# Kernel optimization log

Hardware: AMD Instinct MI355X
Metric: run time of the kernel (lower is better)

Reference implementation:

```python
import jax, jax.numpy as jnp
import numpy as np

EMBED_DIM = 1280
NUM_HEADS = 16
HEAD_DIM = EMBED_DIM // NUM_HEADS  # 80
SCALE = HEAD_DIM ** -0.5
BATCH = 16
SEQ = 1024


def setup_inputs() -> dict:
    key = jax.random.key(0)
    k1, k2, k3, k4, k5 = jax.random.split(key, 5)
    return {
        "hidden_states": jax.random.normal(k1, (BATCH, SEQ, EMBED_DIM), dtype=jnp.float32),
        "w_qkv": jax.random.normal(k2, (EMBED_DIM, 3 * EMBED_DIM), dtype=jnp.float32) * (EMBED_DIM ** -0.5),
        "b_qkv": jax.random.normal(k3, (3 * EMBED_DIM,), dtype=jnp.float32) * 0.02,
        "w_proj": jax.random.normal(k4, (EMBED_DIM, EMBED_DIM), dtype=jnp.float32) * (EMBED_DIM ** -0.5),
        "b_proj": jax.random.normal(k5, (EMBED_DIM,), dtype=jnp.float32) * 0.02,
    }


def reference(hidden_states, w_qkv, b_qkv, w_proj, b_proj):
    b, s, e = hidden_states.shape
    # QKV projection: [b, s, 3e] -> [3, b, h, s, d]
    qkv = hidden_states @ w_qkv + b_qkv
    qkv = qkv.reshape(b, s, 3, NUM_HEADS, HEAD_DIM).transpose(2, 0, 3, 1, 4)
    q, k, v = qkv[0], qkv[1], qkv[2]
    # full attention matrix [b, h, s, s]
    attn = jnp.einsum("bhqd,bhkd->bhqk", q, k) * SCALE
    attn = jax.nn.softmax(attn, axis=-1)
    # dropout p=0.0 (eval): identity
    out = jnp.einsum("bhqk,bhkd->bhqd", attn, v)
    out = out.transpose(0, 2, 1, 3).reshape(b, s, e)
    return out @ w_proj + b_proj
```

## Files before the change

kernel.cpp:

```cpp
#include <hip/hip_runtime.h>

#define BATCH 16
#define SEQ   1024
#define EMBED 1280
#define NH    16
#define HD    80
#define HDP   96
#define NQKV  3840
#define MTOK  (BATCH*SEQ)
#define SCALE 0.11180339887498948f
#define LOG2E 1.4426950408889634f

#define SK_STRIDE 104
#define SV_STRIDE 72
#define SP_STRIDE 72

typedef _Float16 half8 __attribute__((ext_vector_type(8)));
typedef _Float16 half4 __attribute__((ext_vector_type(4)));
typedef float floatx4 __attribute__((ext_vector_type(4)));

#define GLD_TO_LDS(gp, lp)                                                        \
  __builtin_amdgcn_global_load_lds(                                               \
      (const __attribute__((address_space(1))) void*)(gp),                        \
      (__attribute__((address_space(3))) void*)(lp), 16, 0, 0)

__device__ __forceinline__ float rowmax16(float x) {
#define DPP_MAX(ctrl)                                                             \
  {                                                                               \
    float y = __int_as_float(                                                     \
        __builtin_amdgcn_update_dpp(0, __float_as_int(x), ctrl, 0xF, 0xF, true)); \
    x = fmaxf(x, y);                                                              \
  }
  DPP_MAX(0xB1);
  DPP_MAX(0x4E);
  DPP_MAX(0x141);
  DPP_MAX(0x140);
#undef DPP_MAX
  return x;
}

__global__ void cvt_f32_to_f16(const float4* __restrict__ in, _Float16* __restrict__ out, int n4) {
  int i = blockIdx.x * blockDim.x + threadIdx.x;
  if (i < n4) {
    float4 v = in[i];
    half4 h;
    h[0] = (_Float16)v.x; h[1] = (_Float16)v.y; h[2] = (_Float16)v.z; h[3] = (_Float16)v.w;
    *(half4*)(out + (size_t)i * 4) = h;
  }
}

template <int N>
__global__ void cvt_transpose_f16(const float* __restrict__ in, _Float16* __restrict__ out) {
  __shared__ float tile[32][33];
  const int tx = threadIdx.x & 31, ty = threadIdx.x >> 5;
  const int k0 = blockIdx.y * 32;
  const int n0 = blockIdx.x * 32;
#pragma unroll
  for (int j = 0; j < 4; ++j)
    tile[ty + 8 * j][tx] = in[(size_t)(k0 + ty + 8 * j) * N + n0 + tx];
  __syncthreads();
#pragma unroll
  for (int j = 0; j < 4; ++j)
    out[(size_t)(n0 + ty + 8 * j) * 1280 + k0 + tx] = (_Float16)tile[tx][ty + 8 * j];
}


#define STAGE_A(H, T, D)                                                           \
  do {                                                                             \
    GLD_TO_LDS(aSrc0 + (size_t)((H) * 128) * 1280 + (T) * 64,                      \
               &sA[D][((H) * 128 + wave * 16) * 64]);                              \
    GLD_TO_LDS(aSrc0 + (size_t)((H) * 128 + 8) * 1280 + (T) * 64,                  \
               &sA[D][((H) * 128 + wave * 16 + 8) * 64]);                          \
  } while (0)

#define STAGE_B(H, T, D)                                                           \
  do {                                                                             \
    GLD_TO_LDS(bSrc0 + (size_t)((H) * 128) * 1280 + (T) * 64,                      \
               &sB[D][((H) * 128 + wave * 16) * 64]);                              \
    GLD_TO_LDS(bSrc0 + (size_t)((H) * 128 + 8) * 1280 + (T) * 64,                  \
               &sB[D][((H) * 128 + wave * 16 + 8) * 64]);                          \
  } while (0)

#define LDS_FRAG(P, ROWB, FR, KK) (*(const half8*)((P) + ((ROWB) + (FR) * 16) * 64 + cofs[KK]))

#define MFMA_Q(MIB, NIB)                                                           \
  _Pragma("unroll") for (int mi = 0; mi < 4; ++mi)                                 \
    _Pragma("unroll") for (int ni = 0; ni < 2; ++ni)                               \
      _Pragma("unroll") for (int kk = 0; kk < 2; ++kk)                             \
        acc[(MIB) + mi][(NIB) + ni] = __builtin_amdgcn_mfma_f32_16x16x32_f16(      \
            af[mi][kk], bf[(NIB) + ni][kk], acc[(MIB) + mi][(NIB) + ni], 0, 0, 0)

#define GBODY(T, D, S1, S2, VNSTR)                                                 \
  {                                                                                \
    const _Float16* pA = &sA[D][0];                                                \
    const _Float16* pB = &sB[D][0];                                                \
                         \
    _Pragma("unroll") for (int mi = 0; mi < 4; ++mi)                               \
      _Pragma("unroll") for (int kk = 0; kk < 2; ++kk)                             \
        af[mi][kk] = LDS_FRAG(pA, rA, mi, kk);                                     \
    _Pragma("unroll") for (int ni = 0; ni < 2; ++ni)                               \
      _Pragma("unroll") for (int kk = 0; kk < 2; ++kk)                             \
        bf[ni][kk] = LDS_FRAG(pB, rB, ni, kk);                                     \
    if (S1) { STAGE_A(1, (T) + 1, (D) ^ 1); }                                      \
    __builtin_amdgcn_s_barrier();                                                  \
    asm volatile("s_waitcnt lgkmcnt(0)" ::: "memory");                             \
    __builtin_amdgcn_s_setprio(1);                                                 \
    MFMA_Q(0, 0);                                                                  \
    __builtin_amdgcn_s_setprio(0);                                                 \
    __builtin_amdgcn_s_barrier();                                                  \
                                                   \
    _Pragma("unroll") for (int ni = 0; ni < 2; ++ni)                               \
      _Pragma("unroll") for (int kk = 0; kk < 2; ++kk)                             \
        bf[2 + ni][kk] = LDS_FRAG(pB, rB, 2 + ni, kk);                             \
    __builtin_amdgcn_s_barrier();                                                  \
    asm volatile("s_waitcnt lgkmcnt(0)" ::: "memory");                             \
    __builtin_amdgcn_s_setprio(1);                                                 \
    MFMA_Q(0, 2);                                                                  \
    __builtin_amdgcn_s_setprio(0);                                                 \
    __builtin_amdgcn_s_barrier();                                                  \
                                  \
    _Pragma("unroll") for (int mi = 0; mi < 4; ++mi)                               \
      _Pragma("unroll") for (int kk = 0; kk < 2; ++kk)                             \
        af[mi][kk] = LDS_FRAG(pA, rA, 4 + mi, kk);                                 \
    if (S2) { STAGE_B(0, (T) + 2, (D)); }                                          \
    __builtin_amdgcn_s_barrier();                                                  \
    asm volatile("s_waitcnt lgkmcnt(0)" ::: "memory");                             \
    __builtin_amdgcn_s_setprio(1);                                                 \
    MFMA_Q(4, 0);                                                                  \
    __builtin_amdgcn_s_setprio(0);                                                 \
    __builtin_amdgcn_s_barrier();                                                  \
            \
    if (S2) { STAGE_A(0, (T) + 2, (D)); STAGE_B(1, (T) + 2, (D)); }                \
    __builtin_amdgcn_s_barrier();                                                  \
    __builtin_amdgcn_s_setprio(1);                                                 \
    MFMA_Q(4, 2);                                                                  \
    __builtin_amdgcn_s_setprio(0);                                                 \
    asm volatile("s_waitcnt " VNSTR ::: "memory");                                 \
    __builtin_amdgcn_s_barrier();                                                  \
  }

template <int MODE>
__global__ __launch_bounds__(512, 2)
void gemm256(const _Float16* __restrict__ A, const _Float16* __restrict__ Bt,
             const float* __restrict__ bias,
             _Float16* __restrict__ q_pad, _Float16* __restrict__ k_pad,
             _Float16* __restrict__ v_t, float* __restrict__ outf) {
  __shared__ __align__(16) _Float16 sA[2][256 * 64];
  __shared__ __align__(16) _Float16 sB[2][256 * 64];

  const int tid = threadIdx.x;
  const int wave = tid >> 6, lane = tid & 63, quad = lane >> 4, r16 = lane & 15;
  const int wm = wave >> 2, wn = wave & 3;

  const int pid = blockIdx.x;
  const int xcd = pid & 7, local = pid >> 3;
  const int mt = xcd * 8 + (local & 7);
  const int nt = local >> 3;
  const int m0 = mt * 256, n0 = nt * 256;

  const int l8 = lane >> 3, cg = (lane & 7) ^ l8;
  const _Float16* aSrc0 = A + ((size_t)m0 + wave * 16 + l8) * 1280 + cg * 8;
  const _Float16* bSrc0 = Bt + ((size_t)n0 + wave * 16 + l8) * 1280 + cg * 8;

  const int rA = wm * 128 + r16;
  const int rB = wn * 64 + r16;
  const int cofs[2] = { ((0 + quad) ^ (r16 & 7)) * 8, ((4 + quad) ^ (r16 & 7)) * 8 };

  floatx4 acc[8][4] = {};
  half8 af[4][2], bf[4][2];

  STAGE_A(0, 0, 0); STAGE_A(1, 0, 0); STAGE_B(0, 0, 0); STAGE_B(1, 0, 0);
  STAGE_B(0, 1, 1); STAGE_A(0, 1, 1); STAGE_B(1, 1, 1);
  asm volatile("s_waitcnt vmcnt(6)" ::: "memory");
  __builtin_amdgcn_s_barrier();

  for (int it = 0; it < 9; ++it) {
    GBODY(2 * it, 0, true, true, "vmcnt(6)");
    GBODY(2 * it + 1, 1, true, true, "vmcnt(6)");
  }
  GBODY(18, 0, true, false, "vmcnt(0)");
  GBODY(19, 1, false, false, "vmcnt(0)");

  if (MODE == 1) {
#pragma unroll
    for (int mi = 0; mi < 8; ++mi)
#pragma unroll
      for (int ni = 0; ni < 4; ++ni) {
        int n = n0 + wn * 64 + ni * 16 + r16;
        float bv = bias[n];
#pragma unroll
        for (int r = 0; r < 4; ++r) {
          int m = m0 + wm * 128 + mi * 16 + quad * 4 + r;
          outf[(size_t)m * EMBED + n] = acc[mi][ni][r] + bv;
        }
      }
  } else {
#pragma unroll
    for (int mi = 0; mi < 8; ++mi)
#pragma unroll
      for (int ni = 0; ni < 4; ++ni) {
        int n = n0 + wn * 64 + ni * 16 + r16;
        float bv = bias[n];
        int which = n / 1280;
        int rem = n - which * 1280;
        int h = rem / 80;
        int d = rem - h * 80;
#pragma unroll
        for (int r = 0; r < 4; ++r) {
          int m = m0 + wm * 128 + mi * 16 + quad * 4 + r;
          int b = m >> 10, s = m & 1023;
          int bh = b * NH + h;
          _Float16 val = (_Float16)(acc[mi][ni][r] + bv);
          if (which == 0) {
            q_pad[((size_t)bh * SEQ + s) * HDP + d] = val;
            if (d < 16) q_pad[((size_t)bh * SEQ + s) * HDP + 80 + d] = (_Float16)0.f;
          } else if (which == 1) {
            k_pad[((size_t)bh * SEQ + s) * HDP + d] = val;
            if (d < 16) k_pad[((size_t)bh * SEQ + s) * HDP + 80 + d] = (_Float16)0.f;
          } else {
            v_t[((size_t)bh * HD + d) * SEQ + s] = val;
          }
        }
      }
  }
}

__global__ __launch_bounds__(256, 2)
void attn_kernel(const _Float16* __restrict__ q_pad, const _Float16* __restrict__ k_pad,
                 const _Float16* __restrict__ v_t, _Float16* __restrict__ attn_out) {
  __shared__ __align__(16) _Float16 sK[64 * SK_STRIDE];
  __shared__ __align__(16) _Float16 sV[96 * SV_STRIDE];
  __shared__ __align__(16) _Float16 sP[4][16 * SP_STRIDE];

  const int tid = threadIdx.x;
  const int wave = tid >> 6, lane = tid & 63, quad = lane >> 4, r16 = lane & 15;
  const int bh = blockIdx.x >> 3;
  const int q0 = (blockIdx.x & 7) * 128;

  if (tid < 128) {
    int row = 80 + (tid >> 3), col = (tid & 7) * 8;
    half8 z;
#pragma unroll
    for (int j = 0; j < 8; ++j) z[j] = (row == 80) ? (_Float16)1.f : (_Float16)0.f;
    *(half8*)(sV + row * SV_STRIDE + col) = z;
  }

  half8 qf[2][3];
#pragma unroll
  for (int mi = 0; mi < 2; ++mi) {
    const _Float16* qb = q_pad + ((size_t)bh * SEQ + q0 + wave * 32 + mi * 16 + r16) * HDP;
#pragma unroll
    for (int kq = 0; kq < 3; ++kq) {
      half8 q = *(const half8*)(qb + kq * 32 + quad * 8);
#pragma unroll
      for (int j = 0; j < 8; ++j) q[j] = q[j] * (_Float16)(SCALE * LOG2E);
      qf[mi][kq] = q;
    }
  }

  int rowK[3], colK[3];
#pragma unroll
  for (int i = 0; i < 3; ++i) {
    int c = tid + i * 256;
    rowK[i] = c / 12; colK[i] = c - rowK[i] * 12;
  }
  const int rowV0 = tid >> 3, colV0 = tid & 7;
  const _Float16* kgb = k_pad + ((size_t)bh * SEQ) * HDP;
  const _Float16* vgb = v_t + (size_t)bh * HD * SEQ;

  floatx4 o[2][6] = {};
  float mrow[2][4];
#pragma unroll
  for (int mi = 0; mi < 2; ++mi)
#pragma unroll
    for (int r = 0; r < 4; ++r) mrow[mi][r] = -1e30f;

  for (int kt = 0; kt < 16; ++kt) {
    __syncthreads();
    {
      uint4 tk0 = *(const uint4*)(kgb + ((size_t)(kt * 64 + rowK[0])) * HDP + colK[0] * 8);
      uint4 tk1 = *(const uint4*)(kgb + ((size_t)(kt * 64 + rowK[1])) * HDP + colK[1] * 8);
      uint4 tk2 = *(const uint4*)(kgb + ((size_t)(kt * 64 + rowK[2])) * HDP + colK[2] * 8);
      uint4 tv0 = *(const uint4*)(vgb + (size_t)(rowV0) * SEQ + kt * 64 + colV0 * 8);
      uint4 tv1 = *(const uint4*)(vgb + (size_t)(rowV0 + 32) * SEQ + kt * 64 + colV0 * 8);
      uint4 tv2;
      if (tid < 128)
        tv2 = *(const uint4*)(vgb + (size_t)(rowV0 + 64) * SEQ + kt * 64 + colV0 * 8);
      *(uint4*)(sK + rowK[0] * SK_STRIDE + colK[0] * 8) = tk0;
      *(uint4*)(sK + rowK[1] * SK_STRIDE + colK[1] * 8) = tk1;
      *(uint4*)(sK + rowK[2] * SK_STRIDE + colK[2] * 8) = tk2;
      *(uint4*)(sV + (rowV0) * SV_STRIDE + colV0 * 8) = tv0;
      *(uint4*)(sV + (rowV0 + 32) * SV_STRIDE + colV0 * 8) = tv1;
      if (tid < 128)
        *(uint4*)(sV + (rowV0 + 64) * SV_STRIDE + colV0 * 8) = tv2;
    }
    __syncthreads();

    floatx4 sacc[2][4] = {};
#pragma unroll
    for (int ni = 0; ni < 4; ++ni)
#pragma unroll
      for (int kq = 0; kq < 3; ++kq) {
        half8 kf = *(const half8*)(sK + (ni * 16 + r16) * SK_STRIDE + kq * 32 + quad * 8);
#pragma unroll
        for (int mi = 0; mi < 2; ++mi)
          sacc[mi][ni] = __builtin_amdgcn_mfma_f32_16x16x32_f16(qf[mi][kq], kf, sacc[mi][ni], 0, 0, 0);
      }

#pragma unroll
    for (int mi = 0; mi < 2; ++mi)
#pragma unroll
      for (int r = 0; r < 4; ++r) {
        float mx = fmaxf(fmaxf(sacc[mi][0][r], sacc[mi][1][r]),
                         fmaxf(sacc[mi][2][r], sacc[mi][3][r]));
        mx = rowmax16(mx);
        float mnew = fmaxf(mrow[mi][r], mx);
        float alpha = __builtin_amdgcn_exp2f(mrow[mi][r] - mnew);
        mrow[mi][r] = mnew;
#pragma unroll
        for (int ni = 0; ni < 4; ++ni)
          sacc[mi][ni][r] = __builtin_amdgcn_exp2f(sacc[mi][ni][r] - mnew);
#pragma unroll
        for (int di = 0; di < 6; ++di) o[mi][di][r] *= alpha;
      }

#pragma unroll
    for (int mi = 0; mi < 2; ++mi) {
#pragma unroll
      for (int ni = 0; ni < 4; ++ni)
#pragma unroll
        for (int r = 0; r < 4; ++r)
          sP[wave][(quad * 4 + r) * SP_STRIDE + ni * 16 + r16] = (_Float16)sacc[mi][ni][r];
#pragma unroll
      for (int kp = 0; kp < 2; ++kp) {
        half8 pf = *(const half8*)(&sP[wave][r16 * SP_STRIDE + kp * 32 + quad * 8]);
#pragma unroll
        for (int di = 0; di < 6; ++di) {
          half8 vf = *(const half8*)(sV + (di * 16 + r16) * SV_STRIDE + kp * 32 + quad * 8);
          o[mi][di] = __builtin_amdgcn_mfma_f32_16x16x32_f16(pf, vf, o[mi][di], 0, 0, 0);
        }
      }
    }
  }

  const int b = bh >> 4, h = bh & 15;
#pragma unroll
  for (int mi = 0; mi < 2; ++mi)
#pragma unroll
    for (int r = 0; r < 4; ++r) {
      float l = __shfl(o[mi][5][r], lane & 48);
      float inv = 1.0f / l;
      int tok = b * SEQ + q0 + wave * 32 + mi * 16 + quad * 4 + r;
#pragma unroll
      for (int di = 0; di < 5; ++di) {
        int e = h * HD + di * 16 + r16;
        attn_out[(size_t)tok * EMBED + e] = (_Float16)(o[mi][di][r] * inv);
      }
    }
}

extern "C" void kernel_launch(void* const* d_in, const int* in_sizes, int n_in,
                              void* d_out, int out_size, void* d_ws, size_t ws_size,
                              hipStream_t stream) {
  const float* hidden = (const float*)d_in[0];
  const float* w_qkv  = (const float*)d_in[1];
  const float* b_qkv  = (const float*)d_in[2];
  const float* w_proj = (const float*)d_in[3];
  const float* b_proj = (const float*)d_in[4];
  float* out = (float*)d_out;

  char* ws = (char*)d_ws;
  size_t off = 0;
  _Float16* hidden_h = (_Float16*)(ws + off); off += (size_t)MTOK * EMBED * 2;
  _Float16* wqkv_t   = (_Float16*)(ws + off); off += (size_t)NQKV * EMBED * 2;
  _Float16* wproj_t  = (_Float16*)(ws + off); off += (size_t)EMBED * EMBED * 2;
  _Float16* q_pad    = (_Float16*)(ws + off); off += (size_t)BATCH * NH * SEQ * HDP * 2;
  _Float16* k_pad    = (_Float16*)(ws + off); off += (size_t)BATCH * NH * SEQ * HDP * 2;
  _Float16* v_t      = (_Float16*)(ws + off); off += (size_t)BATCH * NH * HD * SEQ * 2;
  _Float16* attn_out = hidden_h;

  {
    int n4 = MTOK * EMBED / 4;
    cvt_f32_to_f16<<<(n4 + 255) / 256, 256, 0, stream>>>((const float4*)hidden, hidden_h, n4);
  }
  cvt_transpose_f16<NQKV><<<dim3(NQKV / 32, 1280 / 32), 256, 0, stream>>>(w_qkv, wqkv_t);
  cvt_transpose_f16<EMBED><<<dim3(EMBED / 32, 1280 / 32), 256, 0, stream>>>(w_proj, wproj_t);

  gemm256<0><<<960, 512, 0, stream>>>(hidden_h, wqkv_t, b_qkv, q_pad, k_pad, v_t, nullptr);

  attn_kernel<<<BATCH * NH * (SEQ / 128), 256, 0, stream>>>(q_pad, k_pad, v_t, attn_out);

  gemm256<1><<<320, 512, 0, stream>>>(attn_out, wproj_t, b_proj, nullptr, nullptr, nullptr, out);
}
```

Baseline: 650.3 us.

## Double-buffer K/V tiles in attention and drop extra GEMM barriers

The attention kernel now keeps two LDS buffers for K and V and prefetches the next tile into registers while the current tile's QK^T MFMAs run. The prefetched tile is written to the other buffer before the softmax, so each iteration needs one __syncthreads instead of two. The GEMM main loop drops several s_barrier and lgkmcnt waits between MFMA quarters, and s_setprio hints are added around the attention MFMAs. Removing the GEMM barriers risks LDS races if the earlier waits were needed for correctness. The extra LDS buffers may also reduce attention occupancy.

```diff
diff --git a/kernel.cpp b/kernel.cpp
--- a/kernel.cpp
+++ b/kernel.cpp
@@ -102,8 +102,6 @@
       _Pragma("unroll") for (int kk = 0; kk < 2; ++kk)                             \
         bf[ni][kk] = LDS_FRAG(pB, rB, ni, kk);                                     \
     if (S1) { STAGE_A(1, (T) + 1, (D) ^ 1); }                                      \
-    __builtin_amdgcn_s_barrier();                                                  \
-    asm volatile("s_waitcnt lgkmcnt(0)" ::: "memory");                             \
     __builtin_amdgcn_s_setprio(1);                                                 \
     MFMA_Q(0, 0);                                                                  \
     __builtin_amdgcn_s_setprio(0);                                                 \
@@ -112,8 +110,6 @@
     _Pragma("unroll") for (int ni = 0; ni < 2; ++ni)                               \
       _Pragma("unroll") for (int kk = 0; kk < 2; ++kk)                             \
         bf[2 + ni][kk] = LDS_FRAG(pB, rB, 2 + ni, kk);                             \
-    __builtin_amdgcn_s_barrier();                                                  \
-    asm volatile("s_waitcnt lgkmcnt(0)" ::: "memory");                             \
     __builtin_amdgcn_s_setprio(1);                                                 \
     MFMA_Q(0, 2);                                                                  \
     __builtin_amdgcn_s_setprio(0);                                                 \
@@ -123,15 +119,12 @@
       _Pragma("unroll") for (int kk = 0; kk < 2; ++kk)                             \
         af[mi][kk] = LDS_FRAG(pA, rA, 4 + mi, kk);                                 \
     if (S2) { STAGE_B(0, (T) + 2, (D)); }                                          \
-    __builtin_amdgcn_s_barrier();                                                  \
-    asm volatile("s_waitcnt lgkmcnt(0)" ::: "memory");                             \
     __builtin_amdgcn_s_setprio(1);                                                 \
     MFMA_Q(4, 0);                                                                  \
     __builtin_amdgcn_s_setprio(0);                                                 \
     __builtin_amdgcn_s_barrier();                                                  \
-            \
+                 \
     if (S2) { STAGE_A(0, (T) + 2, (D)); STAGE_B(1, (T) + 2, (D)); }                \
-    __builtin_amdgcn_s_barrier();                                                  \
     __builtin_amdgcn_s_setprio(1);                                                 \
     MFMA_Q(4, 2);                                                                  \
     __builtin_amdgcn_s_setprio(0);                                                 \
@@ -228,8 +221,8 @@
 __global__ __launch_bounds__(256, 2)
 void attn_kernel(const _Float16* __restrict__ q_pad, const _Float16* __restrict__ k_pad,
                  const _Float16* __restrict__ v_t, _Float16* __restrict__ attn_out) {
-  __shared__ __align__(16) _Float16 sK[64 * SK_STRIDE];
-  __shared__ __align__(16) _Float16 sV[96 * SV_STRIDE];
+  __shared__ __align__(16) _Float16 sK[2][64 * SK_STRIDE];
+  __shared__ __align__(16) _Float16 sV[2][96 * SV_STRIDE];
   __shared__ __align__(16) _Float16 sP[4][16 * SP_STRIDE];
 
   const int tid = threadIdx.x;
@@ -242,7 +235,8 @@
     half8 z;
 #pragma unroll
     for (int j = 0; j < 8; ++j) z[j] = (row == 80) ? (_Float16)1.f : (_Float16)0.f;
-    *(half8*)(sV + row * SV_STRIDE + col) = z;
+    *(half8*)(&sV[0][row * SV_STRIDE + col]) = z;
+    *(half8*)(&sV[1][row * SV_STRIDE + col]) = z;
   }
 
   half8 qf[2][3];
@@ -268,6 +262,23 @@
   const _Float16* kgb = k_pad + ((size_t)bh * SEQ) * HDP;
   const _Float16* vgb = v_t + (size_t)bh * HD * SEQ;
 
+  {
+    uint4 tk0 = *(const uint4*)(kgb + (size_t)(rowK[0]) * HDP + colK[0] * 8);
+    uint4 tk1 = *(const uint4*)(kgb + (size_t)(rowK[1]) * HDP + colK[1] * 8);
+    uint4 tk2 = *(const uint4*)(kgb + (size_t)(rowK[2]) * HDP + colK[2] * 8);
+    uint4 tv0 = *(const uint4*)(vgb + (size_t)(rowV0) * SEQ + colV0 * 8);
+    uint4 tv1 = *(const uint4*)(vgb + (size_t)(rowV0 + 32) * SEQ + colV0 * 8);
+    *(uint4*)(&sK[0][rowK[0] * SK_STRIDE + colK[0] * 8]) = tk0;
+    *(uint4*)(&sK[0][rowK[1] * SK_STRIDE + colK[1] * 8]) = tk1;
+    *(uint4*)(&sK[0][rowK[2] * SK_STRIDE + colK[2] * 8]) = tk2;
+    *(uint4*)(&sV[0][(rowV0)*SV_STRIDE + colV0 * 8]) = tv0;
+    *(uint4*)(&sV[0][(rowV0 + 32) * SV_STRIDE + colV0 * 8]) = tv1;
+    if (tid < 128) {
+      uint4 tv2 = *(const uint4*)(vgb + (size_t)(rowV0 + 64) * SEQ + colV0 * 8);
+      *(uint4*)(&sV[0][(rowV0 + 64) * SV_STRIDE + colV0 * 8]) = tv2;
+    }
+  }
+
   floatx4 o[2][6] = {};
   float mrow[2][4];
 #pragma unroll
@@ -275,37 +286,45 @@
 #pragma unroll
     for (int r = 0; r < 4; ++r) mrow[mi][r] = -1e30f;
 
+  __syncthreads();
+
   for (int kt = 0; kt < 16; ++kt) {
-    __syncthreads();
-    {
-      uint4 tk0 = *(const uint4*)(kgb + ((size_t)(kt * 64 + rowK[0])) * HDP + colK[0] * 8);
-      uint4 tk1 = *(const uint4*)(kgb + ((size_t)(kt * 64 + rowK[1])) * HDP + colK[1] * 8);
-      uint4 tk2 = *(const uint4*)(kgb + ((size_t)(kt * 64 + rowK[2])) * HDP + colK[2] * 8);
-      uint4 tv0 = *(const uint4*)(vgb + (size_t)(rowV0) * SEQ + kt * 64 + colV0 * 8);
-      uint4 tv1 = *(const uint4*)(vgb + (size_t)(rowV0 + 32) * SEQ + kt * 64 + colV0 * 8);
-      uint4 tv2;
+    const int cur = kt & 1, nxt = cur ^ 1;
+
+    uint4 tk0, tk1, tk2, tv0, tv1, tv2;
+    if (kt < 15) {
+      const int kb = (kt + 1) * 64;
+      tk0 = *(const uint4*)(kgb + (size_t)(kb + rowK[0]) * HDP + colK[0] * 8);
+      tk1 = *(const uint4*)(kgb + (size_t)(kb + rowK[1]) * HDP + colK[1] * 8);
+      tk2 = *(const uint4*)(kgb + (size_t)(kb + rowK[2]) * HDP + colK[2] * 8);
+      tv0 = *(const uint4*)(vgb + (size_t)(rowV0)*SEQ + kb + colV0 * 8);
+      tv1 = *(const uint4*)(vgb + (size_t)(rowV0 + 32) * SEQ + kb + colV0 * 8);
       if (tid < 128)
-        tv2 = *(const uint4*)(vgb + (size_t)(rowV0 + 64) * SEQ + kt * 64 + colV0 * 8);
-      *(uint4*)(sK + rowK[0] * SK_STRIDE + colK[0] * 8) = tk0;
-      *(uint4*)(sK + rowK[1] * SK_STRIDE + colK[1] * 8) = tk1;
-      *(uint4*)(sK + rowK[2] * SK_STRIDE + colK[2] * 8) = tk2;
-      *(uint4*)(sV + (rowV0) * SV_STRIDE + colV0 * 8) = tv0;
-      *(uint4*)(sV + (rowV0 + 32) * SV_STRIDE + colV0 * 8) = tv1;
-      if (tid < 128)
-        *(uint4*)(sV + (rowV0 + 64) * SV_STRIDE + colV0 * 8) = tv2;
-    }
-    __syncthreads();
+        tv2 = *(const uint4*)(vgb + (size_t)(rowV0 + 64) * SEQ + kb + colV0 * 8);
+    }
 
     floatx4 sacc[2][4] = {};
+    __builtin_amdgcn_s_setprio(1);
 #pragma unroll
     for (int ni = 0; ni < 4; ++ni)
 #pragma unroll
       for (int kq = 0; kq < 3; ++kq) {
-        half8 kf = *(const half8*)(sK + (ni * 16 + r16) * SK_STRIDE + kq * 32 + quad * 8);
+        half8 kf = *(const half8*)(&sK[cur][(ni * 16 + r16) * SK_STRIDE + kq * 32 + quad * 8]);
 #pragma unroll
         for (int mi = 0; mi < 2; ++mi)
           sacc[mi][ni] = __builtin_amdgcn_mfma_f32_16x16x32_f16(qf[mi][kq], kf, sacc[mi][ni], 0, 0, 0);
       }
+    __builtin_amdgcn_s_setprio(0);
+
+    if (kt < 15) {
+      *(uint4*)(&sK[nxt][rowK[0] * SK_STRIDE + colK[0] * 8]) = tk0;
+      *(uint4*)(&sK[nxt][rowK[1] * SK_STRIDE + colK[1] * 8]) = tk1;
+      *(uint4*)(&sK[nxt][rowK[2] * SK_STRIDE + colK[2] * 8]) = tk2;
+      *(uint4*)(&sV[nxt][(rowV0)*SV_STRIDE + colV0 * 8]) = tv0;
+      *(uint4*)(&sV[nxt][(rowV0 + 32) * SV_STRIDE + colV0 * 8]) = tv1;
+      if (tid < 128)
+        *(uint4*)(&sV[nxt][(rowV0 + 64) * SV_STRIDE + colV0 * 8]) = tv2;
+    }
 
 #pragma unroll
     for (int mi = 0; mi < 2; ++mi)
@@ -334,13 +353,17 @@
 #pragma unroll
       for (int kp = 0; kp < 2; ++kp) {
         half8 pf = *(const half8*)(&sP[wave][r16 * SP_STRIDE + kp * 32 + quad * 8]);
+        __builtin_amdgcn_s_setprio(1);
 #pragma unroll
         for (int di = 0; di < 6; ++di) {
-          half8 vf = *(const half8*)(sV + (di * 16 + r16) * SV_STRIDE + kp * 32 + quad * 8);
+          half8 vf = *(const half8*)(&sV[cur][(di * 16 + r16) * SV_STRIDE + kp * 32 + quad * 8]);
           o[mi][di] = __builtin_amdgcn_mfma_f32_16x16x32_f16(pf, vf, o[mi][di], 0, 0, 0);
         }
-      }
-    }
+        __builtin_amdgcn_s_setprio(0);
+      }
+    }
+
+    __syncthreads();
   }
 
   const int b = bh >> 4, h = bh & 15;
```

Result: faster. 627.1 us (-3.6%).
